# Optimization experiments

Hardware: AMD Instinct MI355X
Metric: run time of the kernel (lower is better)

Reference implementation:

```python
import jax, jax.numpy as jnp
import numpy as np

B, S, H, D = 4, 2048, 16, 64


def setup_inputs() -> dict:
    key = jax.random.key(0)
    k1, k2, k3 = jax.random.split(key, 3)
    qk = jax.random.normal(k1, (B, S, 2, H, D), dtype=jnp.float32)
    v = jax.random.normal(k2, (B, S, H, D), dtype=jnp.float32)
    n = jax.random.normal(k3, (B, S, H), dtype=jnp.float32)
    return {"qk": qk, "v": v, "n": n}


def reference(qk, v, n):
    # qk: (B,S,2,H,D); v: (B,S,H,D); n: (B,S,H)
    q = qk[:, :, 0]  # (B,S,H,D)
    k = qk[:, :, 1]  # (B,S,H,D)
    seqlen = qk.shape[1]
    # causal raw scores: (B,H,T,S)
    scores = jnp.einsum('bthd,bshd->bhts', q, k)
    mask = jnp.tril(jnp.ones((seqlen, seqlen), dtype=scores.dtype))
    # exp normalizer per (b,h,t)
    n_bht = jnp.exp(jnp.transpose(n, (0, 2, 1)))  # (B,H,S)
    attention = scores * mask / n_bht[:, :, :, None]
    # output: (B,T,H,D)
    out = jnp.einsum('bhts,bshd->bthd', attention, v)
    return out
```

## Files before the change

kernel.cpp:

```cpp
#include <hip/hip_runtime.h>
#include <math.h>

#define B_ 4
#define S_ 2048
#define H_ 16
#define D_ 64
#define C_ 128
#define NC_ (S_ / C_)
#define BH_ (B_ * H_)
#define SPLIT_ 4

__global__ __launch_bounds__(256) void kv_chunk_kernel(
    const float* __restrict__ qk, const float* __restrict__ v,
    float* __restrict__ kvbuf)
{
  __shared__ float Kl[C_][D_];
  __shared__ float Vl[C_][D_];
  const int bid = blockIdx.x;
  const int bh = bid / NC_, c = bid % NC_;
  const int b = bh / H_, h = bh % H_;
  const int t0 = c * C_;
  const int tid = threadIdx.x;

  const size_t kbase = (((size_t)b * S_ * 2 + 1) * H_ + h) * D_;
  const size_t vbase = (((size_t)b * S_) * H_ + h) * D_;

  #pragma unroll
  for (int i = 0; i < 8; ++i) {
    int f = tid + i * 256;
    int row = f >> 4, c4 = (f & 15) << 2;
    size_t t = (size_t)t0 + row;
    *reinterpret_cast<float4*>(&Kl[row][c4]) =
        *reinterpret_cast<const float4*>(qk + kbase + t * (2 * H_ * D_) + c4);
    *reinterpret_cast<float4*>(&Vl[row][c4]) =
        *reinterpret_cast<const float4*>(v + vbase + t * (H_ * D_) + c4);
  }
  __syncthreads();

  const int dkt = tid >> 4;
  const int dvt = tid & 15;
  float acc[4][4] = {};
  #pragma unroll 4
  for (int s = 0; s < C_; ++s) {
    float4 k4 = *reinterpret_cast<const float4*>(&Kl[s][dkt * 4]);
    float4 v4 = *reinterpret_cast<const float4*>(&Vl[s][dvt * 4]);
    float kk[4] = {k4.x, k4.y, k4.z, k4.w};
    float vv[4] = {v4.x, v4.y, v4.z, v4.w};
    #pragma unroll
    for (int a = 0; a < 4; ++a)
      #pragma unroll
      for (int e = 0; e < 4; ++e)
        acc[a][e] += kk[a] * vv[e];
  }
  float* outp = kvbuf + (size_t)bid * (D_ * D_);
  #pragma unroll
  for (int a = 0; a < 4; ++a) {
    float4 o = make_float4(acc[a][0], acc[a][1], acc[a][2], acc[a][3]);
    *reinterpret_cast<float4*>(outp + (dkt * 4 + a) * D_ + dvt * 4) = o;
  }
}

__global__ __launch_bounds__(256) void prefix_kernel(float* __restrict__ kvbuf)
{
  const int bid = blockIdx.x;
  const int bh = bid / SPLIT_, part = bid % SPLIT_;
  const size_t off = (size_t)part * 1024 + (size_t)threadIdx.x * 4;
  float4 run = make_float4(0.f, 0.f, 0.f, 0.f);
  for (int c = 0; c < NC_; ++c) {
    float* p = kvbuf + ((size_t)bh * NC_ + c) * (D_ * D_) + off;
    float4 t = *reinterpret_cast<float4*>(p);
    *reinterpret_cast<float4*>(p) = run;
    run.x += t.x; run.y += t.y; run.z += t.z; run.w += t.w;
  }
}

__global__ __launch_bounds__(256) void out_kernel(
    const float* __restrict__ qk, const float* __restrict__ v,
    const float* __restrict__ nrm, const float* __restrict__ kvbuf,
    float* __restrict__ outp)
{
  __shared__ float Qt[D_][C_];
  __shared__ float Ml[D_][D_];
  __shared__ float Kt[D_][32];
  __shared__ float Vl[32][D_];
  __shared__ float Sc[C_][32];

  const int bid = blockIdx.x;
  const int bh = bid / NC_, c = bid % NC_;
  const int b = bh / H_, h = bh % H_;
  const int t0 = c * C_;
  const int tid = threadIdx.x;

  {
    const int t = tid >> 1;
    const int d0 = (tid & 1) * 32;
    const float* qrow =
        qk + ((((size_t)b * S_ + t0 + t) * 2 + 0) * H_ + h) * D_ + d0;
    float tmp[32];
    #pragma unroll
    for (int i = 0; i < 8; ++i) {
      float4 x = *reinterpret_cast<const float4*>(qrow + i * 4);
      tmp[i*4+0] = x.x; tmp[i*4+1] = x.y; tmp[i*4+2] = x.z; tmp[i*4+3] = x.w;
    }
    #pragma unroll
    for (int i = 0; i < 32; ++i) Qt[d0 + i][t] = tmp[i];
  }
  {
    const float* msrc = kvbuf + (size_t)bid * (D_ * D_);
    float* mdst = &Ml[0][0];
    #pragma unroll
    for (int i = 0; i < 4; ++i) {
      int f = (tid + i * 256) * 4;
      *reinterpret_cast<float4*>(mdst + f) =
          *reinterpret_cast<const float4*>(msrc + f);
    }
  }
  __syncthreads();

  const int tg = tid >> 4;
  const int dvg = tid & 15;
  const int tb = tg * 8;
  float acc[8][4] = {};

  if (c > 0) {
    #pragma unroll 4
    for (int dk = 0; dk < D_; ++dk) {
      float4 m4 = *reinterpret_cast<const float4*>(&Ml[dk][dvg * 4]);
      float4 qa = *reinterpret_cast<const float4*>(&Qt[dk][tb]);
      float4 qb = *reinterpret_cast<const float4*>(&Qt[dk][tb + 4]);
      float qv[8] = {qa.x, qa.y, qa.z, qa.w, qb.x, qb.y, qb.z, qb.w};
      float mv[4] = {m4.x, m4.y, m4.z, m4.w};
      #pragma unroll
      for (int i = 0; i < 8; ++i)
        #pragma unroll
        for (int j = 0; j < 4; ++j)
          acc[i][j] += qv[i] * mv[j];
    }
  }

  const int sp = dvg * 2;
  for (int j = 0; j < 4; ++j) {
    __syncthreads();
    {
      const int s = tid >> 3;
      const int d0 = (tid & 7) * 8;
      const size_t sg = (size_t)t0 + j * 32 + s;
      const float* krow =
          qk + ((((size_t)b * S_ + sg) * 2 + 1) * H_ + h) * D_ + d0;
      const float* vrow = v + (((size_t)b * S_ + sg) * H_ + h) * D_ + d0;
      float4 ka = *reinterpret_cast<const float4*>(krow);
      float4 kb = *reinterpret_cast<const float4*>(krow + 4);
      Kt[d0+0][s] = ka.x; Kt[d0+1][s] = ka.y; Kt[d0+2][s] = ka.z; Kt[d0+3][s] = ka.w;
      Kt[d0+4][s] = kb.x; Kt[d0+5][s] = kb.y; Kt[d0+6][s] = kb.z; Kt[d0+7][s] = kb.w;
      *reinterpret_cast<float4*>(&Vl[s][d0]) =
          *reinterpret_cast<const float4*>(vrow);
      *reinterpret_cast<float4*>(&Vl[s][d0 + 4]) =
          *reinterpret_cast<const float4*>(vrow + 4);
    }
    __syncthreads();
    const bool active = (j * 32 <= tb + 7);
    if (active) {
      float sc0[8] = {}, sc1[8] = {};
      #pragma unroll 4
      for (int d = 0; d < D_; ++d) {
        float4 qa = *reinterpret_cast<const float4*>(&Qt[d][tb]);
        float4 qb = *reinterpret_cast<const float4*>(&Qt[d][tb + 4]);
        float2 k2 = *reinterpret_cast<const float2*>(&Kt[d][sp]);
        float qv[8] = {qa.x, qa.y, qa.z, qa.w, qb.x, qb.y, qb.z, qb.w};
        #pragma unroll
        for (int i = 0; i < 8; ++i) {
          sc0[i] += qv[i] * k2.x;
          sc1[i] += qv[i] * k2.y;
        }
      }
      #pragma unroll
      for (int i = 0; i < 8; ++i) {
        int tl = tb + i;
        float2 w;
        w.x = (j * 32 + sp     <= tl) ? sc0[i] : 0.f;
        w.y = (j * 32 + sp + 1 <= tl) ? sc1[i] : 0.f;
        *reinterpret_cast<float2*>(&Sc[tl][sp]) = w;
      }
    }
    __syncthreads();
    if (active) {
      #pragma unroll 2
      for (int q4 = 0; q4 < 8; ++q4) {
        float4 v0 = *reinterpret_cast<const float4*>(&Vl[q4*4+0][dvg*4]);
        float4 v1 = *reinterpret_cast<const float4*>(&Vl[q4*4+1][dvg*4]);
        float4 v2 = *reinterpret_cast<const float4*>(&Vl[q4*4+2][dvg*4]);
        float4 v3 = *reinterpret_cast<const float4*>(&Vl[q4*4+3][dvg*4]);
        #pragma unroll
        for (int i = 0; i < 8; ++i) {
          float4 s4 = *reinterpret_cast<const float4*>(&Sc[tb + i][q4*4]);
          acc[i][0] += s4.x*v0.x + s4.y*v1.x + s4.z*v2.x + s4.w*v3.x;
          acc[i][1] += s4.x*v0.y + s4.y*v1.y + s4.z*v2.y + s4.w*v3.y;
          acc[i][2] += s4.x*v0.z + s4.y*v1.z + s4.z*v2.z + s4.w*v3.z;
          acc[i][3] += s4.x*v0.w + s4.y*v1.w + s4.z*v2.w + s4.w*v3.w;
        }
      }
    }
  }

  #pragma unroll
  for (int i = 0; i < 8; ++i) {
    const size_t t = (size_t)t0 + tb + i;
    float nv = nrm[((size_t)b * S_ + t) * H_ + h];
    float inv = expf(-nv);
    float4 o = make_float4(acc[i][0]*inv, acc[i][1]*inv,
                           acc[i][2]*inv, acc[i][3]*inv);
    *reinterpret_cast<float4*>(
        outp + (((size_t)b * S_ + t) * H_ + h) * D_ + dvg * 4) = o;
  }
}

extern "C" void kernel_launch(void* const* d_in, const int* in_sizes, int n_in,
                              void* d_out, int out_size, void* d_ws, size_t ws_size,
                              hipStream_t stream) {
  const float* qk  = (const float*)d_in[0];
  const float* v   = (const float*)d_in[1];
  const float* nrm = (const float*)d_in[2];
  float* out = (float*)d_out;
  float* kvbuf = (float*)d_ws;

  kv_chunk_kernel<<<dim3(BH_ * NC_), dim3(256), 0, stream>>>(qk, v, kvbuf);
  prefix_kernel<<<dim3(BH_ * SPLIT_), dim3(256), 0, stream>>>(kvbuf);
  out_kernel<<<dim3(BH_ * NC_), dim3(256), 0, stream>>>(qk, v, nrm, kvbuf, out);
}
```

Before: 224.6 us.

## Replace shared-memory tiled kernels with per-wave register-resident row computations

Both the chunk KV-state kernel and the output kernel drop their shared-memory tiles and barriers. Each wave now owns one (bh, chunk) or one 64-row query tile, and each lane holds a full 64-wide row in registers. K, V and the prefix state are read straight from global memory as wave-uniform broadcast loads. This removes the __syncthreads and the LDS transposes, but it relies heavily on cache hits and needs about 128 VGPRs per lane for accumulators, which risks lower occupancy and more global-load traffic.

```diff
diff --git a/kernel.cpp b/kernel.cpp
--- a/kernel.cpp
+++ b/kernel.cpp
@@ -9,54 +9,53 @@
 #define NC_ (S_ / C_)
 #define BH_ (B_ * H_)
 #define SPLIT_ 4
+#define T_ 64
+#define NT_ (S_ / T_)
 
 __global__ __launch_bounds__(256) void kv_chunk_kernel(
     const float* __restrict__ qk, const float* __restrict__ v,
     float* __restrict__ kvbuf)
 {
-  __shared__ float Kl[C_][D_];
-  __shared__ float Vl[C_][D_];
-  const int bid = blockIdx.x;
-  const int bh = bid / NC_, c = bid % NC_;
-  const int b = bh / H_, h = bh % H_;
+  const int wid = blockIdx.x * 4 + (threadIdx.x >> 6);
+  const int lane = threadIdx.x & 63;
+  const int bh = wid >> 4, c = wid & 15;
+  const int b = bh >> 4, h = bh & 15;
   const int t0 = c * C_;
-  const int tid = threadIdx.x;
 
-  const size_t kbase = (((size_t)b * S_ * 2 + 1) * H_ + h) * D_;
-  const size_t vbase = (((size_t)b * S_) * H_ + h) * D_;
+  const float* kp = qk + ((((size_t)(b * S_ + t0)) * 2 + 1) * H_ + h) * D_;
+  const float* vp = v + (((size_t)(b * S_ + t0)) * H_ + h) * D_;
 
+  float acc[D_];
   #pragma unroll
-  for (int i = 0; i < 8; ++i) {
-    int f = tid + i * 256;
-    int row = f >> 4, c4 = (f & 15) << 2;
-    size_t t = (size_t)t0 + row;
-    *reinterpret_cast<float4*>(&Kl[row][c4]) =
-        *reinterpret_cast<const float4*>(qk + kbase + t * (2 * H_ * D_) + c4);
-    *reinterpret_cast<float4*>(&Vl[row][c4]) =
-        *reinterpret_cast<const float4*>(v + vbase + t * (H_ * D_) + c4);
+  for (int i = 0; i < D_; ++i) acc[i] = 0.f;
+
+  #pragma unroll 2
+  for (int s = 0; s < C_; ++s) {
+    const float* kr = kp + (size_t)s * (2 * H_ * D_);
+    const float* vr = vp + (size_t)s * (H_ * D_);
+    float kv_ = kr[lane];
+    #pragma unroll
+    for (int jc = 0; jc < 4; ++jc) {
+      float4 a0 = *reinterpret_cast<const float4*>(vr + jc * 16 + 0);
+      float4 a1 = *reinterpret_cast<const float4*>(vr + jc * 16 + 4);
+      float4 a2 = *reinterpret_cast<const float4*>(vr + jc * 16 + 8);
+      float4 a3 = *reinterpret_cast<const float4*>(vr + jc * 16 + 12);
+      acc[jc*16+ 0] += kv_ * a0.x; acc[jc*16+ 1] += kv_ * a0.y;
+      acc[jc*16+ 2] += kv_ * a0.z; acc[jc*16+ 3] += kv_ * a0.w;
+      acc[jc*16+ 4] += kv_ * a1.x; acc[jc*16+ 5] += kv_ * a1.y;
+      acc[jc*16+ 6] += kv_ * a1.z; acc[jc*16+ 7] += kv_ * a1.w;
+      acc[jc*16+ 8] += kv_ * a2.x; acc[jc*16+ 9] += kv_ * a2.y;
+      acc[jc*16+10] += kv_ * a2.z; acc[jc*16+11] += kv_ * a2.w;
+      acc[jc*16+12] += kv_ * a3.x; acc[jc*16+13] += kv_ * a3.y;
+      acc[jc*16+14] += kv_ * a3.z; acc[jc*16+15] += kv_ * a3.w;
+    }
   }
-  __syncthreads();
 
-  const int dkt = tid >> 4;
-  const int dvt = tid & 15;
-  float acc[4][4] = {};
-  #pragma unroll 4
-  for (int s = 0; s < C_; ++s) {
-    float4 k4 = *reinterpret_cast<const float4*>(&Kl[s][dkt * 4]);
-    float4 v4 = *reinterpret_cast<const float4*>(&Vl[s][dvt * 4]);
-    float kk[4] = {k4.x, k4.y, k4.z, k4.w};
-    float vv[4] = {v4.x, v4.y, v4.z, v4.w};
-    #pragma unroll
-    for (int a = 0; a < 4; ++a)
-      #pragma unroll
-      for (int e = 0; e < 4; ++e)
-        acc[a][e] += kk[a] * vv[e];
-  }
-  float* outp = kvbuf + (size_t)bid * (D_ * D_);
+  float* op = kvbuf + (size_t)wid * (D_ * D_) + (size_t)lane * D_;
   #pragma unroll
-  for (int a = 0; a < 4; ++a) {
-    float4 o = make_float4(acc[a][0], acc[a][1], acc[a][2], acc[a][3]);
-    *reinterpret_cast<float4*>(outp + (dkt * 4 + a) * D_ + dvt * 4) = o;
+  for (int j = 0; j < 16; ++j) {
+    *reinterpret_cast<float4*>(op + 4 * j) =
+        make_float4(acc[4*j], acc[4*j+1], acc[4*j+2], acc[4*j+3]);
   }
 }
 
@@ -79,138 +78,85 @@
     const float* __restrict__ nrm, const float* __restrict__ kvbuf,
     float* __restrict__ outp)
 {
-  __shared__ float Qt[D_][C_];
-  __shared__ float Ml[D_][D_];
-  __shared__ float Kt[D_][32];
-  __shared__ float Vl[32][D_];
-  __shared__ float Sc[C_][32];
+  const int wid = blockIdx.x * 4 + (threadIdx.x >> 6);
+  const int lane = threadIdx.x & 63;
+  const int bh = wid >> 5;
+  const int tt = wid & 31;
+  const int b = bh >> 4, h = bh & 15;
+  const int t0 = tt * T_;
+  const int c = tt >> 1;
+  const int t = t0 + lane;
 
-  const int bid = blockIdx.x;
-  const int bh = bid / NC_, c = bid % NC_;
-  const int b = bh / H_, h = bh % H_;
-  const int t0 = c * C_;
-  const int tid = threadIdx.x;
+  const float* qrow = qk + ((((size_t)(b * S_ + t)) * 2 + 0) * H_ + h) * D_;
 
-  {
-    const int t = tid >> 1;
-    const int d0 = (tid & 1) * 32;
-    const float* qrow =
-        qk + ((((size_t)b * S_ + t0 + t) * 2 + 0) * H_ + h) * D_ + d0;
-    float tmp[32];
-    #pragma unroll
-    for (int i = 0; i < 8; ++i) {
-      float4 x = *reinterpret_cast<const float4*>(qrow + i * 4);
-      tmp[i*4+0] = x.x; tmp[i*4+1] = x.y; tmp[i*4+2] = x.z; tmp[i*4+3] = x.w;
-    }
-    #pragma unroll
-    for (int i = 0; i < 32; ++i) Qt[d0 + i][t] = tmp[i];
+  float q[D_];
+  #pragma unroll
+  for (int j = 0; j < 16; ++j) {
+    float4 x = *reinterpret_cast<const float4*>(qrow + 4 * j);
+    q[4*j] = x.x; q[4*j+1] = x.y; q[4*j+2] = x.z; q[4*j+3] = x.w;
   }
-  {
-    const float* msrc = kvbuf + (size_t)bid * (D_ * D_);
-    float* mdst = &Ml[0][0];
-    #pragma unroll
-    for (int i = 0; i < 4; ++i) {
-      int f = (tid + i * 256) * 4;
-      *reinterpret_cast<float4*>(mdst + f) =
-          *reinterpret_cast<const float4*>(msrc + f);
-    }
-  }
-  __syncthreads();
-
-  const int tg = tid >> 4;
-  const int dvg = tid & 15;
-  const int tb = tg * 8;
-  float acc[8][4] = {};
+  float o[D_];
+  #pragma unroll
+  for (int i = 0; i < D_; ++i) o[i] = 0.f;
 
   if (c > 0) {
-    #pragma unroll 4
-    for (int dk = 0; dk < D_; ++dk) {
-      float4 m4 = *reinterpret_cast<const float4*>(&Ml[dk][dvg * 4]);
-      float4 qa = *reinterpret_cast<const float4*>(&Qt[dk][tb]);
-      float4 qb = *reinterpret_cast<const float4*>(&Qt[dk][tb + 4]);
-      float qv[8] = {qa.x, qa.y, qa.z, qa.w, qb.x, qb.y, qb.z, qb.w};
-      float mv[4] = {m4.x, m4.y, m4.z, m4.w};
+    const float* M = kvbuf + ((size_t)bh * NC_ + c) * (D_ * D_);
+    for (int kq = 0; kq < 16; ++kq) {
+      float4 q4 = *reinterpret_cast<const float4*>(qrow + 4 * kq);
+      const float* mr = M + (size_t)kq * 4 * D_;
       #pragma unroll
-      for (int i = 0; i < 8; ++i)
+      for (int i = 0; i < 4; ++i) {
+        float qv = (i == 0) ? q4.x : (i == 1) ? q4.y : (i == 2) ? q4.z : q4.w;
+        const float* mri = mr + i * D_;
         #pragma unroll
-        for (int j = 0; j < 4; ++j)
-          acc[i][j] += qv[i] * mv[j];
-    }
-  }
-
-  const int sp = dvg * 2;
-  for (int j = 0; j < 4; ++j) {
-    __syncthreads();
-    {
-      const int s = tid >> 3;
-      const int d0 = (tid & 7) * 8;
-      const size_t sg = (size_t)t0 + j * 32 + s;
-      const float* krow =
-          qk + ((((size_t)b * S_ + sg) * 2 + 1) * H_ + h) * D_ + d0;
-      const float* vrow = v + (((size_t)b * S_ + sg) * H_ + h) * D_ + d0;
-      float4 ka = *reinterpret_cast<const float4*>(krow);
-      float4 kb = *reinterpret_cast<const float4*>(krow + 4);
-      Kt[d0+0][s] = ka.x; Kt[d0+1][s] = ka.y; Kt[d0+2][s] = ka.z; Kt[d0+3][s] = ka.w;
-      Kt[d0+4][s] = kb.x; Kt[d0+5][s] = kb.y; Kt[d0+6][s] = kb.z; Kt[d0+7][s] = kb.w;
-      *reinterpret_cast<float4*>(&Vl[s][d0]) =
-          *reinterpret_cast<const float4*>(vrow);
-      *reinterpret_cast<float4*>(&Vl[s][d0 + 4]) =
-          *reinterpret_cast<const float4*>(vrow + 4);
-    }
-    __syncthreads();
-    const bool active = (j * 32 <= tb + 7);
-    if (active) {
-      float sc0[8] = {}, sc1[8] = {};
-      #pragma unroll 4
-      for (int d = 0; d < D_; ++d) {
-        float4 qa = *reinterpret_cast<const float4*>(&Qt[d][tb]);
-        float4 qb = *reinterpret_cast<const float4*>(&Qt[d][tb + 4]);
-        float2 k2 = *reinterpret_cast<const float2*>(&Kt[d][sp]);
-        float qv[8] = {qa.x, qa.y, qa.z, qa.w, qb.x, qb.y, qb.z, qb.w};
-        #pragma unroll
-        for (int i = 0; i < 8; ++i) {
-          sc0[i] += qv[i] * k2.x;
-          sc1[i] += qv[i] * k2.y;
-        }
-      }
-      #pragma unroll
-      for (int i = 0; i < 8; ++i) {
-        int tl = tb + i;
-        float2 w;
-        w.x = (j * 32 + sp     <= tl) ? sc0[i] : 0.f;
-        w.y = (j * 32 + sp + 1 <= tl) ? sc1[i] : 0.f;
-        *reinterpret_cast<float2*>(&Sc[tl][sp]) = w;
-      }
-    }
-    __syncthreads();
-    if (active) {
-      #pragma unroll 2
-      for (int q4 = 0; q4 < 8; ++q4) {
-        float4 v0 = *reinterpret_cast<const float4*>(&Vl[q4*4+0][dvg*4]);
-        float4 v1 = *reinterpret_cast<const float4*>(&Vl[q4*4+1][dvg*4]);
-        float4 v2 = *reinterpret_cast<const float4*>(&Vl[q4*4+2][dvg*4]);
-        float4 v3 = *reinterpret_cast<const float4*>(&Vl[q4*4+3][dvg*4]);
-        #pragma unroll
-        for (int i = 0; i < 8; ++i) {
-          float4 s4 = *reinterpret_cast<const float4*>(&Sc[tb + i][q4*4]);
-          acc[i][0] += s4.x*v0.x + s4.y*v1.x + s4.z*v2.x + s4.w*v3.x;
-          acc[i][1] += s4.x*v0.y + s4.y*v1.y + s4.z*v2.y + s4.w*v3.y;
-          acc[i][2] += s4.x*v0.z + s4.y*v1.z + s4.z*v2.z + s4.w*v3.z;
-          acc[i][3] += s4.x*v0.w + s4.y*v1.w + s4.z*v2.w + s4.w*v3.w;
+        for (int j = 0; j < 16; ++j) {
+          float4 m4 = *reinterpret_cast<const float4*>(mri + 4 * j);
+          o[4*j]   += qv * m4.x;
+          o[4*j+1] += qv * m4.y;
+          o[4*j+2] += qv * m4.z;
+          o[4*j+3] += qv * m4.w;
         }
       }
     }
   }
 
+  const int s_lo = c * C_;
+  const int s_hi = t0 + T_;
+  const float* kbase2 = qk + ((((size_t)b * S_) * 2 + 1) * H_ + h) * D_;
+  const float* vbase2 = v + (((size_t)b * S_) * H_ + h) * D_;
+
+  #pragma unroll 2
+  for (int s = s_lo; s < s_hi; ++s) {
+    const float* kr = kbase2 + (size_t)s * (2 * H_ * D_);
+    float p0 = 0.f, p1 = 0.f, p2 = 0.f, p3 = 0.f;
+    #pragma unroll
+    for (int j = 0; j < 16; ++j) {
+      float4 k4 = *reinterpret_cast<const float4*>(kr + 4 * j);
+      p0 += q[4*j]   * k4.x;
+      p1 += q[4*j+1] * k4.y;
+      p2 += q[4*j+2] * k4.z;
+      p3 += q[4*j+3] * k4.w;
+    }
+    float sc = (p0 + p1) + (p2 + p3);
+    sc = (s <= t) ? sc : 0.f;
+    const float* vr = vbase2 + (size_t)s * (H_ * D_);
+    #pragma unroll
+    for (int j = 0; j < 16; ++j) {
+      float4 v4 = *reinterpret_cast<const float4*>(vr + 4 * j);
+      o[4*j]   += sc * v4.x;
+      o[4*j+1] += sc * v4.y;
+      o[4*j+2] += sc * v4.z;
+      o[4*j+3] += sc * v4.w;
+    }
+  }
+
+  float nv = nrm[((size_t)(b * S_ + t)) * H_ + h];
+  float inv = expf(-nv);
+  float* op = outp + (((size_t)(b * S_ + t)) * H_ + h) * D_;
   #pragma unroll
-  for (int i = 0; i < 8; ++i) {
-    const size_t t = (size_t)t0 + tb + i;
-    float nv = nrm[((size_t)b * S_ + t) * H_ + h];
-    float inv = expf(-nv);
-    float4 o = make_float4(acc[i][0]*inv, acc[i][1]*inv,
-                           acc[i][2]*inv, acc[i][3]*inv);
-    *reinterpret_cast<float4*>(
-        outp + (((size_t)b * S_ + t) * H_ + h) * D_ + dvg * 4) = o;
+  for (int j = 0; j < 16; ++j) {
+    *reinterpret_cast<float4*>(op + 4 * j) =
+        make_float4(o[4*j]*inv, o[4*j+1]*inv, o[4*j+2]*inv, o[4*j+3]*inv);
   }
 }
 
@@ -223,7 +169,7 @@
   float* out = (float*)d_out;
   float* kvbuf = (float*)d_ws;
 
-  kv_chunk_kernel<<<dim3(BH_ * NC_), dim3(256), 0, stream>>>(qk, v, kvbuf);
+  kv_chunk_kernel<<<dim3(BH_ * NC_ / 4), dim3(256), 0, stream>>>(qk, v, kvbuf);
   prefix_kernel<<<dim3(BH_ * SPLIT_), dim3(256), 0, stream>>>(kvbuf);
-  out_kernel<<<dim3(BH_ * NC_), dim3(256), 0, stream>>>(qk, v, nrm, kvbuf, out);
+  out_kernel<<<dim3(BH_ * NT_ / 4), dim3(256), 0, stream>>>(qk, v, nrm, kvbuf, out);
 }
```

After: 665.0 us. +196.1%, slower.

## Restructure out_kernel LDS layout with XOR swizzles and direct global loads for state and V

Applied to the files above, without the earlier changes.

Q is now stored in a per-thread-group swizzled LDS layout (Qt2 with an XOR key) so the float4 reads avoid bank conflicts. The prefix state matrix and V are read straight from global memory instead of being staged in LDS. The intra-chunk tile grows from 32 to 64 keys, and the score buffer is XOR-swizzled, cutting the loop to two iterations with fewer barriers. This lowers LDS footprint and conflicts, but adds global/L2 traffic and latency for the repeated V and M reads.

```diff
diff --git a/kernel.cpp b/kernel.cpp
--- a/kernel.cpp
+++ b/kernel.cpp
@@ -79,21 +79,24 @@
     const float* __restrict__ nrm, const float* __restrict__ kvbuf,
     float* __restrict__ outp)
 {
-  __shared__ float Qt[D_][C_];
-  __shared__ float Ml[D_][D_];
-  __shared__ float Kt[D_][32];
-  __shared__ float Vl[32][D_];
-  __shared__ float Sc[C_][32];
+  __shared__ float Qt2[16][D_][8];
+  __shared__ float Kt[D_][64];
+  __shared__ float Sc[C_][64];
 
   const int bid = blockIdx.x;
   const int bh = bid / NC_, c = bid % NC_;
   const int b = bh / H_, h = bh % H_;
   const int t0 = c * C_;
   const int tid = threadIdx.x;
+  const int TG = tid >> 4;
+  const int SG = tid & 15;
+  const int tb = TG * 8;
+  const int key = TG & 7;
 
   {
     const int t = tid >> 1;
     const int d0 = (tid & 1) * 32;
+    const int wtg = t >> 3, wrow = t & 7, wkey = wtg & 7;
     const float* qrow =
         qk + ((((size_t)b * S_ + t0 + t) * 2 + 0) * H_ + h) * D_ + d0;
     float tmp[32];
@@ -103,100 +106,97 @@
       tmp[i*4+0] = x.x; tmp[i*4+1] = x.y; tmp[i*4+2] = x.z; tmp[i*4+3] = x.w;
     }
     #pragma unroll
-    for (int i = 0; i < 32; ++i) Qt[d0 + i][t] = tmp[i];
-  }
-  {
-    const float* msrc = kvbuf + (size_t)bid * (D_ * D_);
-    float* mdst = &Ml[0][0];
-    #pragma unroll
-    for (int i = 0; i < 4; ++i) {
-      int f = (tid + i * 256) * 4;
-      *reinterpret_cast<float4*>(mdst + f) =
-          *reinterpret_cast<const float4*>(msrc + f);
-    }
+    for (int i = 0; i < 32; ++i)
+      Qt2[wtg][(d0 + i) ^ wkey][wrow] = tmp[i];
   }
   __syncthreads();
 
-  const int tg = tid >> 4;
-  const int dvg = tid & 15;
-  const int tb = tg * 8;
-  float acc[8][4] = {};
+  float o[8][4] = {};
 
   if (c > 0) {
+    const float* M = kvbuf + ((size_t)bh * NC_ + c) * (D_ * D_);
     #pragma unroll 4
     for (int dk = 0; dk < D_; ++dk) {
-      float4 m4 = *reinterpret_cast<const float4*>(&Ml[dk][dvg * 4]);
-      float4 qa = *reinterpret_cast<const float4*>(&Qt[dk][tb]);
-      float4 qb = *reinterpret_cast<const float4*>(&Qt[dk][tb + 4]);
+      const float* qp = &Qt2[TG][dk ^ key][0];
+      float4 qa = *reinterpret_cast<const float4*>(qp);
+      float4 qb = *reinterpret_cast<const float4*>(qp + 4);
+      float4 m4 = *reinterpret_cast<const float4*>(M + dk * D_ + SG * 4);
       float qv[8] = {qa.x, qa.y, qa.z, qa.w, qb.x, qb.y, qb.z, qb.w};
       float mv[4] = {m4.x, m4.y, m4.z, m4.w};
       #pragma unroll
       for (int i = 0; i < 8; ++i)
         #pragma unroll
-        for (int j = 0; j < 4; ++j)
-          acc[i][j] += qv[i] * mv[j];
-    }
-  }
-
-  const int sp = dvg * 2;
-  for (int j = 0; j < 4; ++j) {
+        for (int jj = 0; jj < 4; ++jj)
+          o[i][jj] += qv[i] * mv[jj];
+    }
+  }
+
+  const float* kbase2 = qk + ((((size_t)b * S_) * 2 + 1) * H_ + h) * D_;
+  const float* vbase2 = v + (((size_t)b * S_) * H_ + h) * D_;
+
+  for (int j = 0; j < 2; ++j) {
+    if (j > 0) __syncthreads();
+    {
+      const int sl = tid >> 2;
+      const int d0 = (tid & 3) * 16;
+      const float* krow = kbase2 + (size_t)(t0 + j * 64 + sl) * (2 * H_ * D_) + d0;
+      #pragma unroll
+      for (int q4 = 0; q4 < 4; ++q4) {
+        float4 kx = *reinterpret_cast<const float4*>(krow + q4 * 4);
+        Kt[d0 + q4*4 + 0][sl] = kx.x;
+        Kt[d0 + q4*4 + 1][sl] = kx.y;
+        Kt[d0 + q4*4 + 2][sl] = kx.z;
+        Kt[d0 + q4*4 + 3][sl] = kx.w;
+      }
+    }
     __syncthreads();
-    {
-      const int s = tid >> 3;
-      const int d0 = (tid & 7) * 8;
-      const size_t sg = (size_t)t0 + j * 32 + s;
-      const float* krow =
-          qk + ((((size_t)b * S_ + sg) * 2 + 1) * H_ + h) * D_ + d0;
-      const float* vrow = v + (((size_t)b * S_ + sg) * H_ + h) * D_ + d0;
-      float4 ka = *reinterpret_cast<const float4*>(krow);
-      float4 kb = *reinterpret_cast<const float4*>(krow + 4);
-      Kt[d0+0][s] = ka.x; Kt[d0+1][s] = ka.y; Kt[d0+2][s] = ka.z; Kt[d0+3][s] = ka.w;
-      Kt[d0+4][s] = kb.x; Kt[d0+5][s] = kb.y; Kt[d0+6][s] = kb.z; Kt[d0+7][s] = kb.w;
-      *reinterpret_cast<float4*>(&Vl[s][d0]) =
-          *reinterpret_cast<const float4*>(vrow);
-      *reinterpret_cast<float4*>(&Vl[s][d0 + 4]) =
-          *reinterpret_cast<const float4*>(vrow + 4);
-    }
-    __syncthreads();
-    const bool active = (j * 32 <= tb + 7);
+
+    const bool active = (tb >= j * 64);
     if (active) {
-      float sc0[8] = {}, sc1[8] = {};
+      float sc[8][4] = {};
       #pragma unroll 4
       for (int d = 0; d < D_; ++d) {
-        float4 qa = *reinterpret_cast<const float4*>(&Qt[d][tb]);
-        float4 qb = *reinterpret_cast<const float4*>(&Qt[d][tb + 4]);
-        float2 k2 = *reinterpret_cast<const float2*>(&Kt[d][sp]);
+        const float* qp = &Qt2[TG][d ^ key][0];
+        float4 qa = *reinterpret_cast<const float4*>(qp);
+        float4 qb = *reinterpret_cast<const float4*>(qp + 4);
+        float4 k4 = *reinterpret_cast<const float4*>(&Kt[d][SG * 4]);
         float qv[8] = {qa.x, qa.y, qa.z, qa.w, qb.x, qb.y, qb.z, qb.w};
+        float kv[4] = {k4.x, k4.y, k4.z, k4.w};
+        #pragma unroll
+        for (int i = 0; i < 8; ++i)
+          #pragma unroll
+          for (int jj = 0; jj < 4; ++jj)
+            sc[i][jj] += qv[i] * kv[jj];
+      }
+      #pragma unroll
+      for (int i = 0; i < 8; ++i) {
+        const int tl = tb + i;
+        float4 w;
+        w.x = (j*64 + SG*4 + 0 <= tl) ? sc[i][0] : 0.f;
+        w.y = (j*64 + SG*4 + 1 <= tl) ? sc[i][1] : 0.f;
+        w.z = (j*64 + SG*4 + 2 <= tl) ? sc[i][2] : 0.f;
+        w.w = (j*64 + SG*4 + 3 <= tl) ? sc[i][3] : 0.f;
+        *reinterpret_cast<float4*>(&Sc[tl][4 * (SG ^ key)]) = w;
+      }
+    }
+    __syncthreads();
+
+    if (active) {
+      #pragma unroll 2
+      for (int sq = 0; sq < 16; ++sq) {
+        const int sg0 = t0 + j * 64 + sq * 4;
+        float4 v0 = *reinterpret_cast<const float4*>(vbase2 + (size_t)(sg0+0) * (H_*D_) + SG*4);
+        float4 v1 = *reinterpret_cast<const float4*>(vbase2 + (size_t)(sg0+1) * (H_*D_) + SG*4);
+        float4 v2 = *reinterpret_cast<const float4*>(vbase2 + (size_t)(sg0+2) * (H_*D_) + SG*4);
+        float4 v3 = *reinterpret_cast<const float4*>(vbase2 + (size_t)(sg0+3) * (H_*D_) + SG*4);
+        const int scol = 4 * (sq ^ key);
         #pragma unroll
         for (int i = 0; i < 8; ++i) {
-          sc0[i] += qv[i] * k2.x;
-          sc1[i] += qv[i] * k2.y;
-        }
-      }
-      #pragma unroll
-      for (int i = 0; i < 8; ++i) {
-        int tl = tb + i;
-        float2 w;
-        w.x = (j * 32 + sp     <= tl) ? sc0[i] : 0.f;
-        w.y = (j * 32 + sp + 1 <= tl) ? sc1[i] : 0.f;
-        *reinterpret_cast<float2*>(&Sc[tl][sp]) = w;
-      }
-    }
-    __syncthreads();
-    if (active) {
-      #pragma unroll 2
-      for (int q4 = 0; q4 < 8; ++q4) {
-        float4 v0 = *reinterpret_cast<const float4*>(&Vl[q4*4+0][dvg*4]);
-        float4 v1 = *reinterpret_cast<const float4*>(&Vl[q4*4+1][dvg*4]);
-        float4 v2 = *reinterpret_cast<const float4*>(&Vl[q4*4+2][dvg*4]);
-        float4 v3 = *reinterpret_cast<const float4*>(&Vl[q4*4+3][dvg*4]);
-        #pragma unroll
-        for (int i = 0; i < 8; ++i) {
-          float4 s4 = *reinterpret_cast<const float4*>(&Sc[tb + i][q4*4]);
-          acc[i][0] += s4.x*v0.x + s4.y*v1.x + s4.z*v2.x + s4.w*v3.x;
-          acc[i][1] += s4.x*v0.y + s4.y*v1.y + s4.z*v2.y + s4.w*v3.y;
-          acc[i][2] += s4.x*v0.z + s4.y*v1.z + s4.z*v2.z + s4.w*v3.z;
-          acc[i][3] += s4.x*v0.w + s4.y*v1.w + s4.z*v2.w + s4.w*v3.w;
+          float4 s4 = *reinterpret_cast<const float4*>(&Sc[tb + i][scol]);
+          o[i][0] += s4.x*v0.x + s4.y*v1.x + s4.z*v2.x + s4.w*v3.x;
+          o[i][1] += s4.x*v0.y + s4.y*v1.y + s4.z*v2.y + s4.w*v3.y;
+          o[i][2] += s4.x*v0.z + s4.y*v1.z + s4.z*v2.z + s4.w*v3.z;
+          o[i][3] += s4.x*v0.w + s4.y*v1.w + s4.z*v2.w + s4.w*v3.w;
         }
       }
     }
@@ -207,10 +207,9 @@
     const size_t t = (size_t)t0 + tb + i;
     float nv = nrm[((size_t)b * S_ + t) * H_ + h];
     float inv = expf(-nv);
-    float4 o = make_float4(acc[i][0]*inv, acc[i][1]*inv,
-                           acc[i][2]*inv, acc[i][3]*inv);
+    float4 ov = make_float4(o[i][0]*inv, o[i][1]*inv, o[i][2]*inv, o[i][3]*inv);
     *reinterpret_cast<float4*>(
-        outp + (((size_t)b * S_ + t) * H_ + h) * D_ + dvg * 4) = o;
+        outp + (((size_t)b * S_ + t) * H_ + h) * D_ + SG * 4) = ov;
   }
 }
 
```

Result: faster. 207.9 us (-7.4%).
